# Performance work log

Hardware: AMD Instinct MI355X
Metric: run time of the kernel (lower is better)

The kernel has to match this reference:

```python
import jax, jax.numpy as jnp
import numpy as np

N_NODES = 50000
N_EDGES = 1600000
IN_DIM = 128
OUT_DIM = 64
NEG_SLOPE = 0.2


def setup_inputs() -> dict:
    key = jax.random.key(0)
    k1, k2, k3, k4, k5, k6 = jax.random.split(key, 6)
    in_feat = jax.random.normal(k1, (N_NODES, IN_DIM), dtype=jnp.float32)
    edge_list = jax.random.randint(k2, (2, N_EDGES), 0, N_NODES, dtype=jnp.int64)
    # GATConv params (heads=1): linear weight (no bias), att_src, att_dst, out bias
    W = jax.random.normal(k3, (IN_DIM, OUT_DIM), dtype=jnp.float32) / np.sqrt(IN_DIM)
    a_src = jax.random.normal(k4, (OUT_DIM,), dtype=jnp.float32) / np.sqrt(OUT_DIM)
    a_dst = jax.random.normal(k5, (OUT_DIM,), dtype=jnp.float32) / np.sqrt(OUT_DIM)
    bias = jax.random.normal(k6, (OUT_DIM,), dtype=jnp.float32) * 0.01
    return {"in_feat": in_feat, "edge_list": edge_list, "W": W,
            "a_src": a_src, "a_dst": a_dst, "bias": bias}


def reference(in_feat, edge_list, W, a_src, a_dst, bias):
    # Linear transform: [N, F_in] -> [N, F_out]
    x = in_feat @ W
    src, dst = edge_list[0], edge_list[1]
    # Per-node attention halves, gathered per edge
    alpha_src = x @ a_src  # [N]
    alpha_dst = x @ a_dst  # [N]
    e = alpha_src[src] + alpha_dst[dst]                      # [E]
    e = jnp.where(e > 0, e, NEG_SLOPE * e)                   # leaky_relu
    # Segment softmax over destination node
    e_max = jax.ops.segment_max(e, dst, num_segments=N_NODES)  # [N]
    e_exp = jnp.exp(e - e_max[dst])                          # [E]
    denom = jax.ops.segment_sum(e_exp, dst, num_segments=N_NODES)  # [N]
    alpha = e_exp / (denom[dst] + 1e-16)                     # [E]
    # Weighted scatter-add of source messages into destinations
    msg = x[src] * alpha[:, None]                            # [E, F_out]
    out = jax.ops.segment_sum(msg, dst, num_segments=N_NODES)  # [N, F_out]
    return out + bias
```

## Files before the change

kernel.cpp:

```cpp
#include <hip/hip_runtime.h>
#include <hip/hip_fp16.h>
#include <math.h>

#define IN_DIM 128
#define OUT_DIM 64
#define NEG_SLOPE 0.2f
#define PART_CH 6144
#define PART_RPT 12
#define PBINS 400
#define PBUCK_CAP 5120
#define BUCK_NODES 32
#define BUCK_CAP 1536
#define BG_RPT 20

typedef __attribute__((ext_vector_type(8))) short bf16x8;
typedef __attribute__((ext_vector_type(4))) float f32x4;

__device__ inline unsigned bf16u(float f) {
    unsigned u = __float_as_uint(f);
    return (u + 0x7fffu + ((u >> 16) & 1u)) >> 16;
}

__device__ inline bf16x8 ldfrag(const ushort* p) {
    union { uint2 u2[2]; bf16x8 v; } u;
    u.u2[0] = *(const uint2*)p;
    u.u2[1] = *(const uint2*)(p + 16);
    return u.v;
}

__global__ __launch_bounds__(256) void k_gemm(
        const float* __restrict__ feat, const float* __restrict__ W,
        const float* __restrict__ a_src, const float* __restrict__ a_dst,
        ushort* __restrict__ xb, float* __restrict__ asrc,
        float* __restrict__ adst, int* __restrict__ gcur, int N) {
    __shared__ ushort fA[64][136];
    __shared__ ushort wB[64][136];
    int t = threadIdx.x;
    int row0 = blockIdx.x << 6;

    if (blockIdx.x == 0) {
        gcur[t] = 0;
        gcur[t + 256] = 0;
    }

    {
        const float4* Wv = (const float4*)W;
#pragma unroll
        for (int j = 0; j < 8; ++j) {
            int i = t + 256 * j;
            float4 wv = Wv[i];
            int k = i >> 4, c0 = (i & 15) << 2;
            wB[c0 + 0][k] = (ushort)bf16u(wv.x);
            wB[c0 + 1][k] = (ushort)bf16u(wv.y);
            wB[c0 + 2][k] = (ushort)bf16u(wv.z);
            wB[c0 + 3][k] = (ushort)bf16u(wv.w);
        }
    }
    {
        int nrow = N - row0; if (nrow > 64) nrow = 64;
        int nv = nrow << 5;
        const float4* fv = (const float4*)(feat + (size_t)row0 * IN_DIM);
#pragma unroll
        for (int j = 0; j < 8; ++j) {
            int i = t + 256 * j;
            int row = i >> 5, k0 = (i & 31) << 2;
            ushort4 b;
            if (i < nv) {
                float4 f = fv[i];
                b = make_ushort4((ushort)bf16u(f.x), (ushort)bf16u(f.y),
                                 (ushort)bf16u(f.z), (ushort)bf16u(f.w));
            } else {
                b = make_ushort4(0, 0, 0, 0);
            }
            *(ushort4*)&fA[row][k0] = b;
        }
    }
    __syncthreads();

    int lane = t & 63, w = t >> 6;
    int col16 = lane & 15, kg = lane >> 4;
    int ar = (w << 4) + col16;
    f32x4 zero = {0.f, 0.f, 0.f, 0.f};
    f32x4 acc[4] = {zero, zero, zero, zero};

#pragma unroll
    for (int ks = 0; ks < 4; ++ks) {
        int K0 = (ks << 5) + (kg << 2);
        bf16x8 a = ldfrag(&fA[ar][K0]);
#pragma unroll
        for (int ct = 0; ct < 4; ++ct) {
            bf16x8 b = ldfrag(&wB[(ct << 4) + col16][K0]);
            acc[ct] = __builtin_amdgcn_mfma_f32_16x16x32_bf16(a, b, acc[ct], 0, 0, 0);
        }
    }

    float as[4], ad[4];
#pragma unroll
    for (int ct = 0; ct < 4; ++ct) {
        as[ct] = a_src[(ct << 4) + col16];
        ad[ct] = a_dst[(ct << 4) + col16];
    }
#pragma unroll
    for (int reg = 0; reg < 4; ++reg) {
        int row = row0 + (w << 4) + (kg << 2) + reg;
        float ps = acc[0][reg] * as[0] + acc[1][reg] * as[1] +
                   acc[2][reg] * as[2] + acc[3][reg] * as[3];
        float pd = acc[0][reg] * ad[0] + acc[1][reg] * ad[1] +
                   acc[2][reg] * ad[2] + acc[3][reg] * ad[3];
#pragma unroll
        for (int off = 1; off < 16; off <<= 1) {
            ps += __shfl_xor(ps, off);
            pd += __shfl_xor(pd, off);
        }
        if (row < N) {
            ushort* xp = xb + ((size_t)row << 6) + col16;
            xp[0]  = (ushort)bf16u(acc[0][reg]);
            xp[16] = (ushort)bf16u(acc[1][reg]);
            xp[32] = (ushort)bf16u(acc[2][reg]);
            xp[48] = (ushort)bf16u(acc[3][reg]);
            if (col16 == 0) { asrc[row] = ps; adst[row] = pd; }
        }
    }
}

__global__ __launch_bounds__(512) void k_part(const int* __restrict__ el,
                                              int* __restrict__ gcur,
                                              unsigned* __restrict__ grecs,
                                              int E) {
    __shared__ unsigned srt[PART_CH];
    __shared__ int hist[PBINS], nbeg[PBINS], lbase[PBINS];
    __shared__ int wsum[8];
    int t = threadIdx.x;
    int start = blockIdx.x * PART_CH;
    int len = E - start < PART_CH ? E - start : PART_CH;
    const int* srcp = el + start;
    const int* dstp = el + E + start;

    for (int i = t; i < PBINS; i += 512) hist[i] = 0;
    __syncthreads();

    int dreg[PART_RPT], rreg[PART_RPT];
#pragma unroll
    for (int j = 0; j < PART_RPT; ++j) {
        int i = t + 512 * j;
        if (i < len) {
            int d = dstp[i];
            dreg[j] = d;
            rreg[j] = atomicAdd(&hist[d >> 7], 1);
        }
    }
    __syncthreads();

    int lane = t & 63, wv = t >> 6;
    int c = t < PBINS ? hist[t] : 0;
    int inc = c;
#pragma unroll
    for (int off = 1; off < 64; off <<= 1) {
        int n = __shfl_up(inc, off);
        if (lane >= off) inc += n;
    }
    if (lane == 63) wsum[wv] = inc;
    __syncthreads();
    int woff = 0;
#pragma unroll
    for (int i = 0; i < 8; ++i) woff += (i < wv) ? wsum[i] : 0;
    if (t < PBINS) {
        int excl = woff + inc - c;
        nbeg[t] = excl;
        if (c) lbase[t] = atomicAdd(&gcur[t], c);
    }
    __syncthreads();

#pragma unroll
    for (int j = 0; j < PART_RPT; ++j) {
        int i = t + 512 * j;
        if (i < len) {
            int sx = srcp[i];
            int d = dreg[j];
            srt[nbeg[d >> 7] + rreg[j]] = (unsigned)sx | ((unsigned)d << 16);
        }
    }
    __syncthreads();

    for (int i = t; i < len; i += 512) {
        unsigned r = srt[i];
        int bn = r >> 23;
        int slot = lbase[bn] + (i - nbeg[bn]);
        if (slot < PBUCK_CAP) grecs[(size_t)bn * PBUCK_CAP + slot] = r;
    }
}

__global__ __launch_bounds__(256) void k_bg(
        const unsigned* __restrict__ grecs, const int* __restrict__ gcur,
        const float* __restrict__ asrc, const float* __restrict__ adst,
        const ushort* __restrict__ xb, const float* __restrict__ bias,
        float* __restrict__ out, int N) {
    __shared__ unsigned srt[BUCK_CAP];
    __shared__ int ncnt[BUCK_NODES], nbeg[BUCK_NODES];
    __shared__ float adst_l[BUCK_NODES];
    int t = threadIdx.x;
    int b = blockIdx.x;
    int parent = b >> 2, q = b & 3;
    int node0 = b << 5;
    int cnt = gcur[parent];
    if (cnt > PBUCK_CAP) cnt = PBUCK_CAP;
    const unsigned* rbase = grecs + (size_t)parent * PBUCK_CAP;

    if (t < BUCK_NODES) {
        ncnt[t] = 0;
        int node = node0 + t;
        adst_l[t] = node < N ? adst[node] : 0.f;
    }
    __syncthreads();

    unsigned rec[BG_RPT];
    int rank[BG_RPT];
#pragma unroll
    for (int j = 0; j < BG_RPT; ++j) {
        rank[j] = -1;
        int i = t + 256 * j;
        if (i < cnt) {
            unsigned r = rbase[i];
            rec[j] = r;
            int loc = (r >> 16) & 127;
            if ((loc >> 5) == q) rank[j] = atomicAdd(&ncnt[loc & 31], 1);
        }
    }
    __syncthreads();
    if (t < 64) {
        int v = t < BUCK_NODES ? ncnt[t] : 0;
        int inc = v;
#pragma unroll
        for (int off = 1; off < BUCK_NODES; off <<= 1) {
            int n = __shfl_up(inc, off);
            if (t >= off) inc += n;
        }
        if (t < BUCK_NODES) nbeg[t] = inc - v;
    }
    __syncthreads();
#pragma unroll
    for (int j = 0; j < BG_RPT; ++j) {
        if (rank[j] >= 0) {
            unsigned r = rec[j];
            int loc = (r >> 16) & 31;
            int s = r & 0xFFFF;
            float e = asrc[s] + adst_l[loc];
            e = e > 0.f ? e : NEG_SLOPE * e;
            float p = __expf(e);
            srt[nbeg[loc] + rank[j]] =
                (unsigned)s | ((unsigned)__half_as_ushort(__float2half(p)) << 16);
        }
    }
    __syncthreads();

    int g = t >> 3, sl = t & 7;
    int node = node0 + g;
    if (node >= N) return;
    const ushort* xsl = xb + (sl << 3);
    int c0 = sl << 3;
    float4 ba = *(const float4*)(bias + c0);
    float4 bb = *(const float4*)(bias + c0 + 4);
    int b0 = nbeg[g], b1 = b0 + ncnt[g];
    float acc[8] = {0.f, 0.f, 0.f, 0.f, 0.f, 0.f, 0.f, 0.f};
    float denom = 0.f;
#pragma unroll 4
    for (int i = b0; i < b1; ++i) {
        unsigned r = srt[i];
        float p = __half2float(__ushort_as_half((unsigned short)(r >> 16)));
        uint4 xv = *(const uint4*)(xsl + ((size_t)(r & 0xFFFF) << 6));
        denom += p;
        acc[0] += p * __uint_as_float(xv.x << 16);
        acc[1] += p * __uint_as_float(xv.x & 0xffff0000u);
        acc[2] += p * __uint_as_float(xv.y << 16);
        acc[3] += p * __uint_as_float(xv.y & 0xffff0000u);
        acc[4] += p * __uint_as_float(xv.z << 16);
        acc[5] += p * __uint_as_float(xv.z & 0xffff0000u);
        acc[6] += p * __uint_as_float(xv.w << 16);
        acc[7] += p * __uint_as_float(xv.w & 0xffff0000u);
    }
    float inv = 1.f / (denom + 1e-16f);
    float4 o0 = make_float4(acc[0] * inv + ba.x, acc[1] * inv + ba.y,
                            acc[2] * inv + ba.z, acc[3] * inv + ba.w);
    float4 o1 = make_float4(acc[4] * inv + bb.x, acc[5] * inv + bb.y,
                            acc[6] * inv + bb.z, acc[7] * inv + bb.w);
    float* orow = out + ((size_t)node << 6) + c0;
    *(float4*)orow = o0;
    *(float4*)(orow + 4) = o1;
}

extern "C" void kernel_launch(void* const* d_in, const int* in_sizes, int n_in,
                              void* d_out, int out_size, void* d_ws, size_t ws_size,
                              hipStream_t stream) {
    const float* feat  = (const float*)d_in[0];
    const int*   el    = (const int*)d_in[1];
    const float* W     = (const float*)d_in[2];
    const float* a_src = (const float*)d_in[3];
    const float* a_dst = (const float*)d_in[4];
    const float* bias  = (const float*)d_in[5];
    float* out = (float*)d_out;

    const int N = in_sizes[0] / IN_DIM;
    const int E = in_sizes[1] / 2;
    const int NPB = (E + PART_CH - 1) / PART_CH;
    const int NPAR = (N + 127) >> 7;
    const int NBUCK = (N + BUCK_NODES - 1) / BUCK_NODES;

    char* ws = (char*)d_ws;
    ushort* xb      = (ushort*)ws;   ws += (size_t)N * OUT_DIM * 2;
    float* asrc     = (float*)ws;    ws += (size_t)N * 4;
    float* adst     = (float*)ws;    ws += (size_t)N * 4;
    int*   gcur     = (int*)ws;      ws += 512 * 4;
    unsigned* grecs = (unsigned*)ws; ws += (size_t)NPAR * PBUCK_CAP * 4;

    k_gemm<<<(N + 63) / 64, 256, 0, stream>>>(feat, W, a_src, a_dst, xb, asrc,
                                              adst, gcur, N);
    k_part<<<NPB, 512, 0, stream>>>(el, gcur, grecs, E);
    k_bg<<<NBUCK, 256, 0, stream>>>(grecs, gcur, asrc, adst, xb, bias, out, N);
}
```

Measured before the change: 64.69 us.

## Fuse GEMM and edge partition kernels into one heterogeneous launch

The GEMM and edge-partition kernels are merged into a single launch whose blocks branch on block index: the first blocks partition edges and the rest compute the linear transform. They share LDS through a union, and GEMM blocks now use 512 threads, each wave covering half the output columns, with the attention dot-products combined through shared memory. Because the two stages are independent, they can overlap on the GPU and one dependent launch gap is removed. In exchange, a separate tiny zeroing kernel is added, and the larger union LDS footprint may lower occupancy.

Result: faster. 59.21 us (median of 2 runs) (-8.5%).

```diff
diff --git a/kernel.cpp b/kernel.cpp
--- a/kernel.cpp
+++ b/kernel.cpp
@@ -28,32 +28,105 @@
     return u.v;
 }
 
-__global__ __launch_bounds__(256) void k_gemm(
+struct SmemG {
+    ushort fA[64][136];
+    ushort wB[64][136];
+    float psum[2][2][64];
+};
+struct SmemP {
+    unsigned srt[PART_CH];
+    int hist[PBINS], nbeg[PBINS], lbase[PBINS];
+    int wsum[8];
+};
+union SmemU { SmemG g; SmemP p; };
+
+__global__ void k_zero(int* __restrict__ gcur) { gcur[threadIdx.x] = 0; }
+
+__global__ __launch_bounds__(512) void k_gp(
         const float* __restrict__ feat, const float* __restrict__ W,
         const float* __restrict__ a_src, const float* __restrict__ a_dst,
-        ushort* __restrict__ xb, float* __restrict__ asrc,
-        float* __restrict__ adst, int* __restrict__ gcur, int N) {
-    __shared__ ushort fA[64][136];
-    __shared__ ushort wB[64][136];
+        const int* __restrict__ el, int* __restrict__ gcur,
+        unsigned* __restrict__ grecs, ushort* __restrict__ xb,
+        float* __restrict__ asrc, float* __restrict__ adst,
+        int N, int E, int npb) {
+    __shared__ SmemU sm;
     int t = threadIdx.x;
-    int row0 = blockIdx.x << 6;
-
-    if (blockIdx.x == 0) {
-        gcur[t] = 0;
-        gcur[t + 256] = 0;
-    }
+
+    if ((int)blockIdx.x < npb) {
+        int start = blockIdx.x * PART_CH;
+        int len = E - start < PART_CH ? E - start : PART_CH;
+        const int* srcp = el + start;
+        const int* dstp = el + E + start;
+
+        for (int i = t; i < PBINS; i += 512) sm.p.hist[i] = 0;
+        __syncthreads();
+
+        int dreg[PART_RPT], rreg[PART_RPT];
+#pragma unroll
+        for (int j = 0; j < PART_RPT; ++j) {
+            int i = t + 512 * j;
+            if (i < len) {
+                int d = dstp[i];
+                dreg[j] = d;
+                rreg[j] = atomicAdd(&sm.p.hist[d >> 7], 1);
+            }
+        }
+        __syncthreads();
+
+        int lane = t & 63, wv = t >> 6;
+        int c = t < PBINS ? sm.p.hist[t] : 0;
+        int inc = c;
+#pragma unroll
+        for (int off = 1; off < 64; off <<= 1) {
+            int n = __shfl_up(inc, off);
+            if (lane >= off) inc += n;
+        }
+        if (lane == 63) sm.p.wsum[wv] = inc;
+        __syncthreads();
+        int woff = 0;
+#pragma unroll
+        for (int i = 0; i < 8; ++i) woff += (i < wv) ? sm.p.wsum[i] : 0;
+        if (t < PBINS) {
+            int excl = woff + inc - c;
+            sm.p.nbeg[t] = excl;
+            if (c) sm.p.lbase[t] = atomicAdd(&gcur[t], c);
+        }
+        __syncthreads();
+
+#pragma unroll
+        for (int j = 0; j < PART_RPT; ++j) {
+            int i = t + 512 * j;
+            if (i < len) {
+                int sx = srcp[i];
+                int d = dreg[j];
+                sm.p.srt[sm.p.nbeg[d >> 7] + rreg[j]] =
+                    (unsigned)sx | ((unsigned)d << 16);
+            }
+        }
+        __syncthreads();
+
+        for (int i = t; i < len; i += 512) {
+            unsigned r = sm.p.srt[i];
+            int bn = r >> 23;
+            int slot = sm.p.lbase[bn] + (i - sm.p.nbeg[bn]);
+            if (slot < PBUCK_CAP) grecs[(size_t)bn * PBUCK_CAP + slot] = r;
+        }
+        return;
+    }
+
+    int row0 = ((int)blockIdx.x - npb) << 6;
 
     {
         const float4* Wv = (const float4*)W;
 #pragma unroll
-        for (int j = 0; j < 8; ++j) {
-            int i = t + 256 * j;
+        for (int j = 0; j < 4; ++j) {
+            int i = t + 512 * j;
             float4 wv = Wv[i];
             int k = i >> 4, c0 = (i & 15) << 2;
-            wB[c0 + 0][k] = (ushort)bf16u(wv.x);
-            wB[c0 + 1][k] = (ushort)bf16u(wv.y);
-            wB[c0 + 2][k] = (ushort)bf16u(wv.z);
-            wB[c0 + 3][k] = (ushort)bf16u(wv.w);
+            sm.g.wB[c0 + 0][k] = (ushort)bf16u(wv.x);
+            sm.g.wB[c0 + 1][k] = (ushort)bf16u(wv.y);
+            sm.g.wB[c0 + 2][k] = (ushort)bf16u(wv.z);
+            sm.g.wB[c0 + 3][k] = (ushort)bf16u(wv.w);
         }
     }
     {
@@ -61,8 +134,8 @@
         int nv = nrow << 5;
         const float4* fv = (const float4*)(feat + (size_t)row0 * IN_DIM);
 #pragma unroll
-        for (int j = 0; j < 8; ++j) {
-            int i = t + 256 * j;
+        for (int j = 0; j < 4; ++j) {
+            int i = t + 512 * j;
             int row = i >> 5, k0 = (i & 31) << 2;
             ushort4 b;
             if (i < nv) {
@@ -72,121 +145,61 @@
             } else {
                 b = make_ushort4(0, 0, 0, 0);
             }
-            *(ushort4*)&fA[row][k0] = b;
+            *(ushort4*)&sm.g.fA[row][k0] = b;
         }
     }
     __syncthreads();
 
     int lane = t & 63, w = t >> 6;
     int col16 = lane & 15, kg = lane >> 4;
-    int ar = (w << 4) + col16;
+    int rg = w & 3, ch = w >> 2;
+    int ar = (rg << 4) + col16;
     f32x4 zero = {0.f, 0.f, 0.f, 0.f};
-    f32x4 acc[4] = {zero, zero, zero, zero};
+    f32x4 acc[2] = {zero, zero};
 
 #pragma unroll
     for (int ks = 0; ks < 4; ++ks) {
         int K0 = (ks << 5) + (kg << 2);
-        bf16x8 a = ldfrag(&fA[ar][K0]);
-#pragma unroll
-        for (int ct = 0; ct < 4; ++ct) {
-            bf16x8 b = ldfrag(&wB[(ct << 4) + col16][K0]);
-            acc[ct] = __builtin_amdgcn_mfma_f32_16x16x32_bf16(a, b, acc[ct], 0, 0, 0);
-        }
-    }
-
-    float as[4], ad[4];
-#pragma unroll
-    for (int ct = 0; ct < 4; ++ct) {
-        as[ct] = a_src[(ct << 4) + col16];
-        ad[ct] = a_dst[(ct << 4) + col16];
-    }
+        bf16x8 a = ldfrag(&sm.g.fA[ar][K0]);
+#pragma unroll
+        for (int j = 0; j < 2; ++j) {
+            bf16x8 b = ldfrag(&sm.g.wB[(((ch << 1) + j) << 4) + col16][K0]);
+            acc[j] = __builtin_amdgcn_mfma_f32_16x16x32_bf16(a, b, acc[j], 0, 0, 0);
+        }
+    }
+
+    float as0 = a_src[((ch << 1) << 4) + col16];
+    float as1 = a_src[(((ch << 1) + 1) << 4) + col16];
+    float ad0 = a_dst[((ch << 1) << 4) + col16];
+    float ad1 = a_dst[(((ch << 1) + 1) << 4) + col16];
 #pragma unroll
     for (int reg = 0; reg < 4; ++reg) {
-        int row = row0 + (w << 4) + (kg << 2) + reg;
-        float ps = acc[0][reg] * as[0] + acc[1][reg] * as[1] +
-                   acc[2][reg] * as[2] + acc[3][reg] * as[3];
-        float pd = acc[0][reg] * ad[0] + acc[1][reg] * ad[1] +
-                   acc[2][reg] * ad[2] + acc[3][reg] * ad[3];
+        int rl = (rg << 4) + (kg << 2) + reg;
+        int row = row0 + rl;
+        float ps = acc[0][reg] * as0 + acc[1][reg] * as1;
+        float pd = acc[0][reg] * ad0 + acc[1][reg] * ad1;
 #pragma unroll
         for (int off = 1; off < 16; off <<= 1) {
             ps += __shfl_xor(ps, off);
             pd += __shfl_xor(pd, off);
         }
         if (row < N) {
-            ushort* xp = xb + ((size_t)row << 6) + col16;
+            ushort* xp = xb + ((size_t)row << 6) + (ch << 5) + col16;
             xp[0]  = (ushort)bf16u(acc[0][reg]);
             xp[16] = (ushort)bf16u(acc[1][reg]);
-            xp[32] = (ushort)bf16u(acc[2][reg]);
-            xp[48] = (ushort)bf16u(acc[3][reg]);
-            if (col16 == 0) { asrc[row] = ps; adst[row] = pd; }
-        }
-    }
-}
-
-__global__ __launch_bounds__(512) void k_part(const int* __restrict__ el,
-                                              int* __restrict__ gcur,
-                                              unsigned* __restrict__ grecs,
-                                              int E) {
-    __shared__ unsigned srt[PART_CH];
-    __shared__ int hist[PBINS], nbeg[PBINS], lbase[PBINS];
-    __shared__ int wsum[8];
-    int t = threadIdx.x;
-    int start = blockIdx.x * PART_CH;
-    int len = E - start < PART_CH ? E - start : PART_CH;
-    const int* srcp = el + start;
-    const int* dstp = el + E + start;
-
-    for (int i = t; i < PBINS; i += 512) hist[i] = 0;
-    __syncthreads();
-
-    int dreg[PART_RPT], rreg[PART_RPT];
-#pragma unroll
-    for (int j = 0; j < PART_RPT; ++j) {
-        int i = t + 512 * j;
-        if (i < len) {
-            int d = dstp[i];
-            dreg[j] = d;
-            rreg[j] = atomicAdd(&hist[d >> 7], 1);
-        }
-    }
-    __syncthreads();
-
-    int lane = t & 63, wv = t >> 6;
-    int c = t < PBINS ? hist[t] : 0;
-    int inc = c;
-#pragma unroll
-    for (int off = 1; off < 64; off <<= 1) {
-        int n = __shfl_up(inc, off);
-        if (lane >= off) inc += n;
-    }
-    if (lane == 63) wsum[wv] = inc;
-    __syncthreads();
-    int woff = 0;
-#pragma unroll
-    for (int i = 0; i < 8; ++i) woff += (i < wv) ? wsum[i] : 0;
-    if (t < PBINS) {
-        int excl = woff + inc - c;
-        nbeg[t] = excl;
-        if (c) lbase[t] = atomicAdd(&gcur[t], c);
-    }
-    __syncthreads();
-
-#pragma unroll
-    for (int j = 0; j < PART_RPT; ++j) {
-        int i = t + 512 * j;
-        if (i < len) {
-            int sx = srcp[i];
-            int d = dreg[j];
-            srt[nbeg[d >> 7] + rreg[j]] = (unsigned)sx | ((unsigned)d << 16);
-        }
-    }
-    __syncthreads();
-
-    for (int i = t; i < len; i += 512) {
-        unsigned r = srt[i];
-        int bn = r >> 23;
-        int slot = lbase[bn] + (i - nbeg[bn]);
-        if (slot < PBUCK_CAP) grecs[(size_t)bn * PBUCK_CAP + slot] = r;
+        }
+        if (col16 == 0) {
+            sm.g.psum[ch][0][rl] = ps;
+            sm.g.psum[ch][1][rl] = pd;
+        }
+    }
+    __syncthreads();
+    if (t < 64) {
+        int row = row0 + t;
+        if (row < N) {
+            asrc[row] = sm.g.psum[0][0][t] + sm.g.psum[1][0][t];
+            adst[row] = sm.g.psum[0][1][t] + sm.g.psum[1][1][t];
+        }
     }
 }
 
@@ -302,6 +315,7 @@
     const int N = in_sizes[0] / IN_DIM;
     const int E = in_sizes[1] / 2;
     const int NPB = (E + PART_CH - 1) / PART_CH;
+    const int GB = (N + 63) / 64;
     const int NPAR = (N + 127) >> 7;
     const int NBUCK = (N + BUCK_NODES - 1) / BUCK_NODES;
 
@@ -312,8 +326,8 @@
     int*   gcur     = (int*)ws;      ws += 512 * 4;
     unsigned* grecs = (unsigned*)ws; ws += (size_t)NPAR * PBUCK_CAP * 4;
 
-    k_gemm<<<(N + 63) / 64, 256, 0, stream>>>(feat, W, a_src, a_dst, xb, asrc,
-                                              adst, gcur, N);
-    k_part<<<NPB, 512, 0, stream>>>(el, gcur, grecs, E);
+    k_zero<<<1, 512, 0, stream>>>(gcur);
+    k_gp<<<NPB + GB, 512, 0, stream>>>(feat, W, a_src, a_dst, el, gcur, grecs,
+                                       xb, asrc, adst, N, E, NPB);
     k_bg<<<NBUCK, 256, 0, stream>>>(grecs, gcur, asrc, adst, xb, bias, out, N);
 }
```
